# Kernel tuning notes

Hardware: AMD Instinct MI355X
Metric: run time of the kernel (lower is better)

The kernel has to match this reference:

```python
import jax, jax.numpy as jnp
import numpy as np

H, C = 3, 64          # heads, out_channels
NEG_SLOPE = 0.2       # PyG GATConv leaky_relu default
LN_EPS = 1e-5


def setup_inputs() -> dict:
    key = jax.random.key(0)
    ks = jax.random.split(key, 20)
    N, E, D_in, edge_dim = 50000, 800000, 64, 5
    g = lambda k, shape: (jax.random.normal(k, shape, dtype=jnp.float32) * 0.1)
    return {
        "x": jax.random.normal(ks[0], (N, D_in), dtype=jnp.float32),
        "edge_attr": jax.random.normal(ks[1], (E, edge_dim), dtype=jnp.float32),
        "lin_w": g(ks[2], (D_in, H * C)),          # GATConv.lin (bias=False)
        "att_src": g(ks[3], (H, C)),
        "att_dst": g(ks[4], (H, C)),
        "lin_edge_w": g(ks[5], (edge_dim, H * C)),  # GATConv.lin_edge (bias=False)
        "att_edge": g(ks[6], (H, C)),
        "gat_bias": jnp.zeros((H * C,), jnp.float32),
        "w1": g(ks[7], (H * C, C)),
        "b1": jnp.zeros((C,), jnp.float32),
        "ln1_g": jnp.ones((C,), jnp.float32),
        "ln1_b": jnp.zeros((C,), jnp.float32),
        "w2": g(ks[8], (C, C)),
        "b2": jnp.zeros((C,), jnp.float32),
        "ln2_g": jnp.ones((C,), jnp.float32),
        "ln2_b": jnp.zeros((C,), jnp.float32),
        "edge_index": jax.random.randint(ks[9], (2, E), 0, N),
    }


def layer_norm(x, g, b):
    m = jnp.mean(x, axis=-1, keepdims=True)
    v = jnp.mean((x - m) ** 2, axis=-1, keepdims=True)
    return (x - m) * jax.lax.rsqrt(v + LN_EPS) * g + b


def gat_conv(x, edge_index, edge_attr, lin_w, att_src, att_dst,
             lin_edge_w, att_edge, gat_bias):
    N = x.shape[0]
    src, dst = edge_index[0], edge_index[1]

    # add_self_loops=True with fill_value='mean': self-loop edge_attr is the
    # per-node mean of incoming edge attributes (0 if node has no in-edges).
    attr_sum = jax.ops.segment_sum(edge_attr, dst, num_segments=N)       # [N, edge_dim]
    cnt = jax.ops.segment_sum(jnp.ones((dst.shape[0],), edge_attr.dtype), dst, num_segments=N)
    loop_attr = attr_sum / jnp.maximum(cnt, 1.0)[:, None]
    loop = jnp.arange(N, dtype=src.dtype)
    src = jnp.concatenate([src, loop])
    dst = jnp.concatenate([dst, loop])
    ea = jnp.concatenate([edge_attr, loop_attr], axis=0)                  # [E2, edge_dim]

    xs = (x @ lin_w).reshape(N, H, C)                                     # [N, H, C]
    a_src = jnp.einsum('nhc,hc->nh', xs, att_src)                         # [N, H]
    a_dst = jnp.einsum('nhc,hc->nh', xs, att_dst)                         # [N, H]
    e = (ea @ lin_edge_w).reshape(-1, H, C)                               # [E2, H, C]
    a_edge = jnp.einsum('ehc,hc->eh', e, att_edge)                        # [E2, H]

    logits = a_src[src] + a_dst[dst] + a_edge                             # [E2, H]
    logits = jnp.where(logits >= 0, logits, NEG_SLOPE * logits)           # leaky_relu

    # segment softmax over incoming edges of each dst node (self loops ensure non-empty)
    lmax = jax.ops.segment_max(logits, dst, num_segments=N)               # [N, H]
    ex = jnp.exp(logits - lmax[dst])
    denom = jax.ops.segment_sum(ex, dst, num_segments=N)                  # [N, H]
    alpha = ex / denom[dst]                                               # [E2, H]

    msgs = alpha[:, :, None] * xs[src]                                    # [E2, H, C]
    out = jax.ops.segment_sum(msgs, dst, num_segments=N)                  # [N, H, C]
    return out.reshape(N, H * C) + gat_bias


def reference(x, edge_attr, lin_w, att_src, att_dst, lin_edge_w, att_edge,
              gat_bias, w1, b1, ln1_g, ln1_b, w2, b2, ln2_g, ln2_b, edge_index):
    x_gat = gat_conv(x, edge_index, edge_attr, lin_w, att_src, att_dst,
                     lin_edge_w, att_edge, gat_bias)
    x_gat = x_gat @ w1 + b1                         # linear1: [N, C]
    x_gat = layer_norm(x + x_gat, ln1_g, ln1_b)     # layerNorm1(x + x_gat)
    lin = x_gat @ w2 + b2                           # linear2
    out = layer_norm(lin + x_gat, ln2_g, ln2_b)     # layerNorm2(lin + x_gat)
    return out                                      # dropout p=0 -> identity
```

## Files before the change

### kernel.cpp

```cpp
#include <hip/hip_runtime.h>


#define HH 3
#define CC 64
#define DIN 64
#define ED 5
#define HC 192
#define NEG_SLOPE 0.2f
#define LN_EPS 1e-5f
#define LOG2E 1.44269504f

typedef __attribute__((ext_vector_type(8))) short bf16x8;
typedef __attribute__((ext_vector_type(4))) float f32x4;

__device__ __forceinline__ float leaky(float l) { return fmaxf(l, NEG_SLOPE * l); }

__device__ __forceinline__ unsigned short f2bf(float f) {
    unsigned u = __float_as_uint(f);
    unsigned r = (u + 0x7FFFu + ((u >> 16) & 1u)) >> 16;
    return (unsigned short)r;
}
__device__ __forceinline__ float bf2f(unsigned short u) {
    return __uint_as_float((unsigned)u << 16);
}
__device__ __forceinline__ float bf_lo(unsigned v) { return __uint_as_float(v << 16); }
__device__ __forceinline__ float bf_hi(unsigned v) { return __uint_as_float(v & 0xFFFF0000u); }

__device__ __forceinline__ bf16x8 pack8(float4 a, float4 b) {
    bf16x8 r;
    r[0] = (short)f2bf(a.x); r[1] = (short)f2bf(a.y);
    r[2] = (short)f2bf(a.z); r[3] = (short)f2bf(a.w);
    r[4] = (short)f2bf(b.x); r[5] = (short)f2bf(b.y);
    r[6] = (short)f2bf(b.z); r[7] = (short)f2bf(b.w);
    return r;
}

#define PREP_TOT (HC*DIN + DIN*HC + CC*CC + CC + ED*HH)
#define PREP_BLOCKS 30
__global__ __launch_bounds__(256) void k_prep_cnt(const float* __restrict__ lin_w,
                                                  const float* __restrict__ w1,
                                                  const float* __restrict__ w2,
                                                  const float* __restrict__ b1,
                                                  const float* __restrict__ gat_bias,
                                                  const float* __restrict__ lin_edge_w,
                                                  const float* __restrict__ att_edge,
                                                  unsigned short* __restrict__ linwt,
                                                  unsigned short* __restrict__ w1t,
                                                  unsigned short* __restrict__ w2t,
                                                  float* __restrict__ b1p,
                                                  float* __restrict__ we,
                                                  const int* __restrict__ ei,
                                                  int* __restrict__ icnt, int E) {
    if (blockIdx.x < PREP_BLOCKS) {
        for (int i = blockIdx.x * 256 + threadIdx.x; i < PREP_TOT; i += PREP_BLOCKS * 256) {
            if (i < HC * DIN) {
                int c = i >> 6, k = i & 63;
                linwt[i] = f2bf(lin_w[k * HC + c]);
            } else if (i < 2 * HC * DIN) {
                int j = i - HC * DIN;
                int c = j / HC, k = j - c * HC;
                w1t[j] = f2bf(w1[k * CC + c]);
            } else if (i < 2 * HC * DIN + CC * CC) {
                int j = i - 2 * HC * DIN;
                int c = j >> 6, k = j & 63;
                w2t[j] = f2bf(w2[k * CC + c]);
            } else if (i < 2 * HC * DIN + CC * CC + CC) {
                int c = i - (2 * HC * DIN + CC * CC);
                float s = b1[c];
                for (int k = 0; k < HC; ++k) s += gat_bias[k] * w1[k * CC + c];
                b1p[c] = s;
            } else {
                int q = i - (2 * HC * DIN + CC * CC + CC);
                int d = q / HH, h = q - d * HH;
                float s = 0.f;
                for (int c = 0; c < CC; ++c)
                    s += lin_edge_w[d * HC + h * CC + c] * att_edge[h * CC + c];
                we[q] = s * LOG2E;
            }
        }
    } else {
        int nb = gridDim.x - PREP_BLOCKS;
        for (int e = (blockIdx.x - PREP_BLOCKS) * 256 + threadIdx.x; e < E; e += nb * 256)
            atomicAdd(&icnt[ei[E + e]], 1);
    }
}

__global__ __launch_bounds__(256) void k_xs(const float* __restrict__ x,
                                            const unsigned short* __restrict__ linwt,
                                            const float* __restrict__ att_src,
                                            const float* __restrict__ att_dst,
                                            unsigned short* __restrict__ xsb,
                                            float* __restrict__ a_src,
                                            float* __restrict__ a_dst,
                                            const int* __restrict__ icnt,
                                            int* __restrict__ gtot,
                                            int* __restrict__ off,
                                            int* __restrict__ cursor,
                                            int N, int nbx) {
    __shared__ int wt[4];
    __shared__ int base_sh;
    if ((int)blockIdx.x >= nbx) {
        int bid = blockIdx.x - nbx;
        int i = bid * 256 + threadIdx.x;
        int lane = threadIdx.x & 63, wid = threadIdx.x >> 6;
        int v = (i < N) ? icnt[i] : 0;
        int incl = v;
        #pragma unroll
        for (int o = 1; o < 64; o <<= 1) {
            int u = __shfl_up(incl, o, 64);
            if (lane >= o) incl += u;
        }
        if (lane == 63) wt[wid] = incl;
        __syncthreads();
        if (threadIdx.x == 0)
            base_sh = atomicAdd(gtot, wt[0] + wt[1] + wt[2] + wt[3]);
        __syncthreads();
        int wpre = 0;
        for (int w2 = 0; w2 < wid; ++w2) wpre += wt[w2];
        int excl = base_sh + wpre + incl - v;
        if (i < N) { off[i] = excl; cursor[i] = excl; }
        return;
    }

    int lane = threadIdx.x & 63, w = threadIdx.x >> 6;
    int l15 = lane & 15, kg = (lane >> 4) * 8;
    int nb = blockIdx.x * 64;
    int arow = nb + w * 16 + l15;
    int arow_c = min(arow, N - 1);

    f32x4 acc[12];
    #pragma unroll
    for (int ct = 0; ct < 12; ++ct) acc[ct] = (f32x4){0.f, 0.f, 0.f, 0.f};

    #pragma unroll
    for (int k0 = 0; k0 < DIN; k0 += 32) {
        const float* ap = x + (size_t)arow_c * DIN + k0 + kg;
        float4 a0 = *(const float4*)ap;
        float4 a1 = *(const float4*)(ap + 4);
        bf16x8 af = pack8(a0, a1);
        #pragma unroll
        for (int ct = 0; ct < 12; ++ct) {
            bf16x8 bf = *(const bf16x8*)(linwt + (size_t)(ct * 16 + l15) * DIN + k0 + kg);
            acc[ct] = __builtin_amdgcn_mfma_f32_16x16x32_bf16(af, bf, acc[ct], 0, 0, 0);
        }
    }

    float asv[12], adv[12];
    #pragma unroll
    for (int ct = 0; ct < 12; ++ct) {
        int c = ct * 16 + l15;
        asv[ct] = att_src[c]; adv[ct] = att_dst[c];
    }

    int rbase = nb + w * 16 + (lane >> 4) * 4;
    #pragma unroll
    for (int j = 0; j < 4; ++j) {
        int r = rbase + j;
        bool ok = r < N;
        float ps0 = 0.f, ps1 = 0.f, ps2 = 0.f, pd0 = 0.f, pd1 = 0.f, pd2 = 0.f;
        #pragma unroll
        for (int ct = 0; ct < 12; ++ct) {
            float v = acc[ct][j];
            float s = v * asv[ct], d = v * adv[ct];
            if (ct < 4)      { ps0 += s; pd0 += d; }
            else if (ct < 8) { ps1 += s; pd1 += d; }
            else             { ps2 += s; pd2 += d; }
        }
        if (ok) {
            unsigned* row32 = (unsigned*)(xsb + (size_t)r * HC);
            #pragma unroll
            for (int ct = 0; ct < 4; ++ct) {
                int c = ct * 16 + l15;
                row32[c] = (unsigned)f2bf(acc[ct][j]) | ((unsigned)f2bf(acc[ct + 4][j]) << 16);
                xsb[(size_t)r * HC + 128 + c] = f2bf(acc[ct + 8][j]);
            }
        }
        #pragma unroll
        for (int o = 1; o < 16; o <<= 1) {
            ps0 += __shfl_xor(ps0, o, 64); pd0 += __shfl_xor(pd0, o, 64);
            ps1 += __shfl_xor(ps1, o, 64); pd1 += __shfl_xor(pd1, o, 64);
            ps2 += __shfl_xor(ps2, o, 64); pd2 += __shfl_xor(pd2, o, 64);
        }
        if (ok && l15 == 0) {
            a_src[r * HH + 0] = ps0 * LOG2E; a_src[r * HH + 1] = ps1 * LOG2E;
            a_src[r * HH + 2] = ps2 * LOG2E;
            a_dst[r * HH + 0] = pd0 * LOG2E; a_dst[r * HH + 1] = pd1 * LOG2E;
            a_dst[r * HH + 2] = pd2 * LOG2E;
        }
    }
}

__global__ __launch_bounds__(256) void k_fill(const float* __restrict__ ea,
                                              const int* __restrict__ ei,
                                              const float* __restrict__ a_src,
                                              const float* __restrict__ a_dst,
                                              const float* __restrict__ we,
                                              int* __restrict__ cursor,
                                              uint4* __restrict__ payload, int E) {
    int e = blockIdx.x * blockDim.x + threadIdx.x;
    if (e >= E) return;
    int s = ei[e], d = ei[E + e];
    int pos = atomicAdd(&cursor[d], 1);
    float attr[ED];
    #pragma unroll
    for (int j = 0; j < ED; ++j) attr[j] = ea[(size_t)e * ED + j];
    float aeh[HH], lp[HH];
    #pragma unroll
    for (int h = 0; h < HH; ++h) {
        float a = 0.f;
        #pragma unroll
        for (int j = 0; j < ED; ++j) a += attr[j] * we[j * HH + h];
        aeh[h] = a;
        lp[h] = a_src[s * HH + h] + a_dst[d * HH + h] + a;
    }
    uint4 pk;
    pk.x = (unsigned)f2bf(lp[0])  | ((unsigned)f2bf(lp[1])  << 16);
    pk.y = (unsigned)f2bf(lp[2])  | ((unsigned)f2bf(aeh[0]) << 16);
    pk.z = (unsigned)f2bf(aeh[1]) | ((unsigned)f2bf(aeh[2]) << 16);
    pk.w = (unsigned)s;
    payload[pos] = pk;
}

__global__ __launch_bounds__(256) void k_gat(const unsigned short* __restrict__ xsb,
                                             const float* __restrict__ a_src,
                                             const float* __restrict__ a_dst,
                                             const int* __restrict__ off,
                                             const int* __restrict__ icnt,
                                             const uint4* __restrict__ payload,
                                             unsigned short* __restrict__ oaccb, int N) {
    __shared__ float4 wbuf[4][64];
    int lane = threadIdx.x & 63;
    int wid  = threadIdx.x >> 6;
    const unsigned* xs32 = (const unsigned*)xsb;
    unsigned c128ml = 128u - (unsigned)lane;
    for (int n = blockIdx.x * 4 + wid; n < N; n += gridDim.x * 4) {
        int beg = off[n];
        int deg = icnt[n];

        float pden0 = 0.f, pden1 = 0.f, pden2 = 0.f;
        float pae0 = 0.f, pae1 = 0.f, pae2 = 0.f;
        float a0A = 0.f, a1A = 0.f, a2A = 0.f;
        float a0B = 0.f, a1B = 0.f, a2B = 0.f;

        for (int c0 = 0; c0 < deg; c0 += 64) {
            int cn = min(deg - c0, 64);
            float w0 = 0.f, w1 = 0.f, w2 = 0.f;
            int src = 0;
            if (lane < cn) {
                uint4 p = payload[beg + c0 + lane];
                w0 = exp2f(leaky(bf_lo(p.x)));
                w1 = exp2f(leaky(bf_hi(p.x)));
                w2 = exp2f(leaky(bf_lo(p.y)));
                pae0 += bf_hi(p.y);
                pae1 += bf_lo(p.z);
                pae2 += bf_hi(p.z);
                pden0 += w0; pden1 += w1; pden2 += w2;
                src = (int)p.w;
            }
            wbuf[wid][lane] = make_float4(w0, w1, w2, __int_as_float(src));
            int i = 0;
            for (; i + 2 <= cn; i += 2) {
                float4 ta = wbuf[wid][i];
                float4 tb = wbuf[wid][i + 1];
                unsigned ia = __umul24((unsigned)__float_as_int(ta.w), 96u) + lane;
                unsigned ib = __umul24((unsigned)__float_as_int(tb.w), 96u) + lane;
                unsigned va = xs32[ia];
                unsigned vb = xs32[ib];
                float xa2 = bf2f(xsb[(ia << 1) + c128ml]);
                float xb2 = bf2f(xsb[(ib << 1) + c128ml]);
                a0A += ta.x * bf_lo(va); a1A += ta.y * bf_hi(va); a2A += ta.z * xa2;
                a0B += tb.x * bf_lo(vb); a1B += tb.y * bf_hi(vb); a2B += tb.z * xb2;
            }
            if (i < cn) {
                float4 ta = wbuf[wid][i];
                unsigned ia = __umul24((unsigned)__float_as_int(ta.w), 96u) + lane;
                unsigned va = xs32[ia];
                a0A += ta.x * bf_lo(va);
                a1A += ta.y * bf_hi(va);
                a2A += ta.z * bf2f(xsb[(ia << 1) + c128ml]);
            }
        }

        #pragma unroll
        for (int o = 32; o; o >>= 1) {
            pden0 += __shfl_xor(pden0, o, 64);
            pden1 += __shfl_xor(pden1, o, 64);
            pden2 += __shfl_xor(pden2, o, 64);
            pae0  += __shfl_xor(pae0, o, 64);
            pae1  += __shfl_xor(pae1, o, 64);
            pae2  += __shfl_xor(pae2, o, 64);
        }

        float dc = fmaxf((float)deg, 1.0f);
        float inv_dc = __builtin_amdgcn_rcpf(dc);
        float sl0 = leaky(a_src[n * HH + 0] + a_dst[n * HH + 0] + pae0 * inv_dc);
        float sl1 = leaky(a_src[n * HH + 1] + a_dst[n * HH + 1] + pae1 * inv_dc);
        float sl2 = leaky(a_src[n * HH + 2] + a_dst[n * HH + 2] + pae2 * inv_dc);
        float e0 = exp2f(sl0), e1 = exp2f(sl1), e2 = exp2f(sl2);
        unsigned ian = __umul24((unsigned)n, 96u) + lane;
        unsigned van = xs32[ian];
        float xn2 = bf2f(xsb[(ian << 1) + c128ml]);
        float r0 = __builtin_amdgcn_rcpf(pden0 + e0);
        float r1 = __builtin_amdgcn_rcpf(pden1 + e1);
        float r2 = __builtin_amdgcn_rcpf(pden2 + e2);
        float acc0 = (a0A + a0B + e0 * bf_lo(van)) * r0;
        float acc1 = (a1A + a1B + e1 * bf_hi(van)) * r1;
        float acc2 = (a2A + a2B + e2 * xn2) * r2;
        size_t nbse = (size_t)n * HC;
        oaccb[nbse + 0 * CC + lane] = f2bf(acc0);
        oaccb[nbse + 1 * CC + lane] = f2bf(acc1);
        oaccb[nbse + 2 * CC + lane] = f2bf(acc2);
    }
}

__global__ __launch_bounds__(256) void k_mlp(const unsigned short* __restrict__ oaccb,
                                             const unsigned short* __restrict__ w1t,
                                             const unsigned short* __restrict__ w2t,
                                             const float* __restrict__ b1p,
                                             const float* __restrict__ x,
                                             const float* __restrict__ g1,
                                             const float* __restrict__ be1,
                                             const float* __restrict__ b2,
                                             const float* __restrict__ g2,
                                             const float* __restrict__ be2,
                                             float* __restrict__ out, int N) {
    __shared__ unsigned short H1[64 * 72];
    int lane = threadIdx.x & 63, w = threadIdx.x >> 6;
    int l15 = lane & 15, kg = (lane >> 4) * 8;
    int nb = blockIdx.x * 64;
    int arow = nb + w * 16 + l15;
    int arow_c = min(arow, N - 1);

    float c_b1[4], c_g1[4], c_be1[4], c_b2[4], c_g2[4], c_be2[4];
    #pragma unroll
    for (int ct = 0; ct < 4; ++ct) {
        int c = ct * 16 + l15;
        c_b1[ct] = b1p[c]; c_g1[ct] = g1[c]; c_be1[ct] = be1[c];
        c_b2[ct] = b2[c];  c_g2[ct] = g2[c]; c_be2[ct] = be2[c];
    }

    f32x4 acc[4];
    #pragma unroll
    for (int ct = 0; ct < 4; ++ct) acc[ct] = (f32x4){0.f, 0.f, 0.f, 0.f};
    #pragma unroll
    for (int k0 = 0; k0 < HC; k0 += 32) {
        bf16x8 af = *(const bf16x8*)(oaccb + (size_t)arow_c * HC + k0 + kg);
        #pragma unroll
        for (int ct = 0; ct < 4; ++ct) {
            bf16x8 bf = *(const bf16x8*)(w1t + (size_t)(ct * 16 + l15) * HC + k0 + kg);
            acc[ct] = __builtin_amdgcn_mfma_f32_16x16x32_bf16(af, bf, acc[ct], 0, 0, 0);
        }
    }

    int rbase = nb + w * 16 + (lane >> 4) * 4;
    int rloc0 = w * 16 + (lane >> 4) * 4;
    float h1v[4][4];
    float y[4][4];
    #pragma unroll
    for (int j = 0; j < 4; ++j) {
        int r = min(rbase + j, N - 1);
        #pragma unroll
        for (int ct = 0; ct < 4; ++ct)
            y[ct][j] = acc[ct][j] + c_b1[ct] + x[(size_t)r * DIN + ct * 16 + l15];
    }
    #pragma unroll
    for (int j = 0; j < 4; ++j) {
        float s = y[0][j] + y[1][j] + y[2][j] + y[3][j];
        #pragma unroll
        for (int o = 1; o < 16; o <<= 1) s += __shfl_xor(s, o, 64);
        float m = s * (1.0f / CC);
        float vs = 0.f;
        #pragma unroll
        for (int ct = 0; ct < 4; ++ct) { float d = y[ct][j] - m; vs += d * d; }
        #pragma unroll
        for (int o = 1; o < 16; o <<= 1) vs += __shfl_xor(vs, o, 64);
        float inv = rsqrtf(vs * (1.0f / CC) + LN_EPS);
        #pragma unroll
        for (int ct = 0; ct < 4; ++ct) {
            float h = (y[ct][j] - m) * inv * c_g1[ct] + c_be1[ct];
            h1v[ct][j] = h;
            H1[(rloc0 + j) * 72 + ct * 16 + l15] = f2bf(h);
        }
    }
    __syncthreads();

    f32x4 acc2[4];
    #pragma unroll
    for (int ct = 0; ct < 4; ++ct) acc2[ct] = (f32x4){0.f, 0.f, 0.f, 0.f};
    #pragma unroll
    for (int k0 = 0; k0 < CC; k0 += 32) {
        bf16x8 af = *(const bf16x8*)&H1[(w * 16 + l15) * 72 + k0 + kg];
        #pragma unroll
        for (int ct = 0; ct < 4; ++ct) {
            bf16x8 bf = *(const bf16x8*)(w2t + (size_t)(ct * 16 + l15) * CC + k0 + kg);
            acc2[ct] = __builtin_amdgcn_mfma_f32_16x16x32_bf16(af, bf, acc2[ct], 0, 0, 0);
        }
    }

    #pragma unroll
    for (int j = 0; j < 4; ++j) {
        float z0 = acc2[0][j] + c_b2[0] + h1v[0][j];
        float z1 = acc2[1][j] + c_b2[1] + h1v[1][j];
        float z2 = acc2[2][j] + c_b2[2] + h1v[2][j];
        float z3 = acc2[3][j] + c_b2[3] + h1v[3][j];
        float s = z0 + z1 + z2 + z3;
        #pragma unroll
        for (int o = 1; o < 16; o <<= 1) s += __shfl_xor(s, o, 64);
        float m = s * (1.0f / CC);
        float d0 = z0 - m, d1 = z1 - m, d2 = z2 - m, d3 = z3 - m;
        float vs = d0 * d0 + d1 * d1 + d2 * d2 + d3 * d3;
        #pragma unroll
        for (int o = 1; o < 16; o <<= 1) vs += __shfl_xor(vs, o, 64);
        float inv = rsqrtf(vs * (1.0f / CC) + LN_EPS);
        int r = rbase + j;
        if (r < N) {
            out[(size_t)r * CC + 0 * 16 + l15] = d0 * inv * c_g2[0] + c_be2[0];
            out[(size_t)r * CC + 1 * 16 + l15] = d1 * inv * c_g2[1] + c_be2[1];
            out[(size_t)r * CC + 2 * 16 + l15] = d2 * inv * c_g2[2] + c_be2[2];
            out[(size_t)r * CC + 3 * 16 + l15] = d3 * inv * c_g2[3] + c_be2[3];
        }
    }
}

extern "C" void kernel_launch(void* const* d_in, const int* in_sizes, int n_in,
                              void* d_out, int out_size, void* d_ws, size_t ws_size,
                              hipStream_t stream) {
    const float* x          = (const float*)d_in[0];
    const float* edge_attr  = (const float*)d_in[1];
    const float* lin_w      = (const float*)d_in[2];
    const float* att_src    = (const float*)d_in[3];
    const float* att_dst    = (const float*)d_in[4];
    const float* lin_edge_w = (const float*)d_in[5];
    const float* att_edge   = (const float*)d_in[6];
    const float* gat_bias   = (const float*)d_in[7];
    const float* w1         = (const float*)d_in[8];
    const float* b1         = (const float*)d_in[9];
    const float* ln1_g      = (const float*)d_in[10];
    const float* ln1_b      = (const float*)d_in[11];
    const float* w2         = (const float*)d_in[12];
    const float* b2         = (const float*)d_in[13];
    const float* ln2_g      = (const float*)d_in[14];
    const float* ln2_b      = (const float*)d_in[15];
    const int*   ei         = (const int*)d_in[16];
    float* out = (float*)d_out;

    const int N = in_sizes[0] / DIN;
    const int E = in_sizes[1] / ED;
    const int nb_scan = (N + 255) / 256;
    const int nbx = (N + 63) / 64;

    char* ws = (char*)d_ws;
    size_t off_b = 0;
    auto alloc = [&](size_t bytes) {
        size_t o = off_b;
        off_b = (off_b + bytes + 255) & ~(size_t)255;
        return o;
    };
    int* icnt = (int*)(ws + alloc((size_t)N * 4));
    int* gtot = (int*)(ws + alloc(4));
    size_t zero_bytes = off_b;
    unsigned short* xsb   = (unsigned short*)(ws + alloc((size_t)N * HC * 2));
    unsigned short* oaccb = (unsigned short*)(ws + alloc((size_t)N * HC * 2));
    float*  a_srcb  = (float*)(ws + alloc((size_t)N * HH * 4));
    float*  a_dstb  = (float*)(ws + alloc((size_t)N * HH * 4));
    int*    offb    = (int*)(ws + alloc((size_t)N * 4));
    int*    cursor  = (int*)(ws + alloc((size_t)N * 4));
    uint4*  payload = (uint4*)(ws + alloc((size_t)E * 16));
    unsigned short* linwt = (unsigned short*)(ws + alloc((size_t)HC * DIN * 2));
    unsigned short* w1t   = (unsigned short*)(ws + alloc((size_t)DIN * HC * 2));
    unsigned short* w2t   = (unsigned short*)(ws + alloc((size_t)CC * CC * 2));
    float* b1p = (float*)(ws + alloc((size_t)CC * 4));
    float* we  = (float*)(ws + alloc((size_t)ED * HH * 4));
    (void)ws_size; (void)n_in; (void)out_size;

    hipMemsetAsync(d_ws, 0, zero_bytes, stream);

    k_prep_cnt<<<PREP_BLOCKS + (E + 255) / 256, 256, 0, stream>>>(
        lin_w, w1, w2, b1, gat_bias, lin_edge_w, att_edge,
        linwt, w1t, w2t, b1p, we, ei, icnt, E);
    k_xs<<<nbx + nb_scan, 256, 0, stream>>>(x, linwt, att_src, att_dst, xsb,
                                            a_srcb, a_dstb, icnt, gtot, offb, cursor,
                                            N, nbx);
    k_fill<<<(E + 255) / 256, 256, 0, stream>>>(edge_attr, ei, a_srcb, a_dstb, we, cursor,
                                                payload, E);
    k_gat<<<(N + 3) / 4, 256, 0, stream>>>(xsb, a_srcb, a_dstb, offb, icnt, payload, oaccb, N);
    k_mlp<<<(N + 63) / 64, 256, 0, stream>>>(oaccb, w1t, w2t, b1p, x,
                                             ln1_g, ln1_b, b2, ln2_g, ln2_b, out, N);
}
```

Baseline: 184.9 us.

## Fuse GAT aggregation with MLP and layer norms in one kernel

```diff
diff --git a/kernel.cpp b/kernel.cpp
--- a/kernel.cpp
+++ b/kernel.cpp
@@ -221,204 +221,190 @@
     payload[pos] = pk;
 }
 
-__global__ __launch_bounds__(256) void k_gat(const unsigned short* __restrict__ xsb,
-                                             const float* __restrict__ a_src,
-                                             const float* __restrict__ a_dst,
-                                             const int* __restrict__ off,
-                                             const int* __restrict__ icnt,
-                                             const uint4* __restrict__ payload,
-                                             unsigned short* __restrict__ oaccb, int N) {
+__global__ __launch_bounds__(256) void k_gatmlp(const unsigned short* __restrict__ xsb,
+                                                const float* __restrict__ a_src,
+                                                const float* __restrict__ a_dst,
+                                                const int* __restrict__ off,
+                                                const int* __restrict__ icnt,
+                                                const uint4* __restrict__ payload,
+                                                const float* __restrict__ x,
+                                                const unsigned short* __restrict__ w1t,
+                                                const unsigned short* __restrict__ w2t,
+                                                const float* __restrict__ b1p,
+                                                const float* __restrict__ g1,
+                                                const float* __restrict__ be1,
+                                                const float* __restrict__ b2,
+                                                const float* __restrict__ g2,
+                                                const float* __restrict__ be2,
+                                                float* __restrict__ out, int N) {
     __shared__ float4 wbuf[4][64];
+    __shared__ unsigned short OA[16 * HC];
+    __shared__ unsigned short H1s[16 * 72];
+    __shared__ float red[2][4][16];
     int lane = threadIdx.x & 63;
     int wid  = threadIdx.x >> 6;
     const unsigned* xs32 = (const unsigned*)xsb;
     unsigned c128ml = 128u - (unsigned)lane;
-    for (int n = blockIdx.x * 4 + wid; n < N; n += gridDim.x * 4) {
-        int beg = off[n];
-        int deg = icnt[n];
-
-        float pden0 = 0.f, pden1 = 0.f, pden2 = 0.f;
-        float pae0 = 0.f, pae1 = 0.f, pae2 = 0.f;
-        float a0A = 0.f, a1A = 0.f, a2A = 0.f;
-        float a0B = 0.f, a1B = 0.f, a2B = 0.f;
-
-        for (int c0 = 0; c0 < deg; c0 += 64) {
-            int cn = min(deg - c0, 64);
-            float w0 = 0.f, w1 = 0.f, w2 = 0.f;
-            int src = 0;
-            if (lane < cn) {
-                uint4 p = payload[beg + c0 + lane];
-                w0 = exp2f(leaky(bf_lo(p.x)));
-                w1 = exp2f(leaky(bf_hi(p.x)));
-                w2 = exp2f(leaky(bf_lo(p.y)));
-                pae0 += bf_hi(p.y);
-                pae1 += bf_lo(p.z);
-                pae2 += bf_hi(p.z);
-                pden0 += w0; pden1 += w1; pden2 += w2;
-                src = (int)p.w;
+    int nb16 = blockIdx.x * 16;
+
+    #pragma unroll 1
+    for (int t = 0; t < 4; ++t) {
+        int row = wid * 4 + t;
+        int n = nb16 + row;
+        if (n < N) {
+            int beg = off[n];
+            int deg = icnt[n];
+            float pden0 = 0.f, pden1 = 0.f, pden2 = 0.f;
+            float pae0 = 0.f, pae1 = 0.f, pae2 = 0.f;
+            float a0A = 0.f, a1A = 0.f, a2A = 0.f;
+            float a0B = 0.f, a1B = 0.f, a2B = 0.f;
+
+            for (int c0 = 0; c0 < deg; c0 += 64) {
+                int cn = min(deg - c0, 64);
+                float w0 = 0.f, w1 = 0.f, w2 = 0.f;
+                int src = 0;
+                if (lane < cn) {
+                    uint4 p = payload[beg + c0 + lane];
+                    w0 = exp2f(leaky(bf_lo(p.x)));
+                    w1 = exp2f(leaky(bf_hi(p.x)));
+                    w2 = exp2f(leaky(bf_lo(p.y)));
+                    pae0 += bf_hi(p.y);
+                    pae1 += bf_lo(p.z);
+                    pae2 += bf_hi(p.z);
+                    pden0 += w0; pden1 += w1; pden2 += w2;
+                    src = (int)p.w;
+                }
+                wbuf[wid][lane] = make_float4(w0, w1, w2, __int_as_float(src));
+                int i = 0;
+                for (; i + 2 <= cn; i += 2) {
+                    float4 ta = wbuf[wid][i];
+                    float4 tb = wbuf[wid][i + 1];
+                    unsigned ia = __umul24((unsigned)__float_as_int(ta.w), 96u) + lane;
+                    unsigned ib = __umul24((unsigned)__float_as_int(tb.w), 96u) + lane;
+                    unsigned va = xs32[ia];
+                    unsigned vb = xs32[ib];
+                    float xa2 = bf2f(xsb[(ia << 1) + c128ml]);
+                    float xb2 = bf2f(xsb[(ib << 1) + c128ml]);
+                    a0A += ta.x * bf_lo(va); a1A += ta.y * bf_hi(va); a2A += ta.z * xa2;
+                    a0B += tb.x * bf_lo(vb); a1B += tb.y * bf_hi(vb); a2B += tb.z * xb2;
+                }
+                if (i < cn) {
+                    float4 ta = wbuf[wid][i];
+                    unsigned ia = __umul24((unsigned)__float_as_int(ta.w), 96u) + lane;
+                    unsigned va = xs32[ia];
+                    a0A += ta.x * bf_lo(va);
+                    a1A += ta.y * bf_hi(va);
+                    a2A += ta.z * bf2f(xsb[(ia << 1) + c128ml]);
+                }
             }
-            wbuf[wid][lane] = make_float4(w0, w1, w2, __int_as_float(src));
-            int i = 0;
-            for (; i + 2 <= cn; i += 2) {
-                float4 ta = wbuf[wid][i];
-                float4 tb = wbuf[wid][i + 1];
-                unsigned ia = __umul24((unsigned)__float_as_int(ta.w), 96u) + lane;
-                unsigned ib = __umul24((unsigned)__float_as_int(tb.w), 96u) + lane;
-                unsigned va = xs32[ia];
-                unsigned vb = xs32[ib];
-                float xa2 = bf2f(xsb[(ia << 1) + c128ml]);
-                float xb2 = bf2f(xsb[(ib << 1) + c128ml]);
-                a0A += ta.x * bf_lo(va); a1A += ta.y * bf_hi(va); a2A += ta.z * xa2;
-                a0B += tb.x * bf_lo(vb); a1B += tb.y * bf_hi(vb); a2B += tb.z * xb2;
+
+            #pragma unroll
+            for (int o = 32; o; o >>= 1) {
+                pden0 += __shfl_xor(pden0, o, 64);
+                pden1 += __shfl_xor(pden1, o, 64);
+                pden2 += __shfl_xor(pden2, o, 64);
+                pae0  += __shfl_xor(pae0, o, 64);
+                pae1  += __shfl_xor(pae1, o, 64);
+                pae2  += __shfl_xor(pae2, o, 64);
             }
-            if (i < cn) {
-                float4 ta = wbuf[wid][i];
-                unsigned ia = __umul24((unsigned)__float_as_int(ta.w), 96u) + lane;
-                unsigned va = xs32[ia];
-                a0A += ta.x * bf_lo(va);
-                a1A += ta.y * bf_hi(va);
-                a2A += ta.z * bf2f(xsb[(ia << 1) + c128ml]);
-            }
-        }
-
-        #pragma unroll
-        for (int o = 32; o; o >>= 1) {
-            pden0 += __shfl_xor(pden0, o, 64);
-            pden1 += __shfl_xor(pden1, o, 64);
-            pden2 += __shfl_xor(pden2, o, 64);
-            pae0  += __shfl_xor(pae0, o, 64);
-            pae1  += __shfl_xor(pae1, o, 64);
-            pae2  += __shfl_xor(pae2, o, 64);
-        }
-
-        float dc = fmaxf((float)deg, 1.0f);
-        float inv_dc = __builtin_amdgcn_rcpf(dc);
-        float sl0 = leaky(a_src[n * HH + 0] + a_dst[n * HH + 0] + pae0 * inv_dc);
-        float sl1 = leaky(a_src[n * HH + 1] + a_dst[n * HH + 1] + pae1 * inv_dc);
-        float sl2 = leaky(a_src[n * HH + 2] + a_dst[n * HH + 2] + pae2 * inv_dc);
-        float e0 = exp2f(sl0), e1 = exp2f(sl1), e2 = exp2f(sl2);
-        unsigned ian = __umul24((unsigned)n, 96u) + lane;
-        unsigned van = xs32[ian];
-        float xn2 = bf2f(xsb[(ian << 1) + c128ml]);
-        float r0 = __builtin_amdgcn_rcpf(pden0 + e0);
-        float r1 = __builtin_amdgcn_rcpf(pden1 + e1);
-        float r2 = __builtin_amdgcn_rcpf(pden2 + e2);
-        float acc0 = (a0A + a0B + e0 * bf_lo(van)) * r0;
-        float acc1 = (a1A + a1B + e1 * bf_hi(van)) * r1;
-        float acc2 = (a2A + a2B + e2 * xn2) * r2;
-        size_t nbse = (size_t)n * HC;
-        oaccb[nbse + 0 * CC + lane] = f2bf(acc0);
-        oaccb[nbse + 1 * CC + lane] = f2bf(acc1);
-        oaccb[nbse + 2 * CC + lane] = f2bf(acc2);
-    }
-}
-
-__global__ __launch_bounds__(256) void k_mlp(const unsigned short* __restrict__ oaccb,
-                                             const unsigned short* __restrict__ w1t,
-                                             const unsigned short* __restrict__ w2t,
-                                             const float* __restrict__ b1p,
-                                             const float* __restrict__ x,
-                                             const float* __restrict__ g1,
-                                             const float* __restrict__ be1,
-                                             const float* __restrict__ b2,
-                                             const float* __restrict__ g2,
-                                             const float* __restrict__ be2,
-                                             float* __restrict__ out, int N) {
-    __shared__ unsigned short H1[64 * 72];
-    int lane = threadIdx.x & 63, w = threadIdx.x >> 6;
+
+            float dc = fmaxf((float)deg, 1.0f);
+            float inv_dc = __builtin_amdgcn_rcpf(dc);
+            float sl0 = leaky(a_src[n * HH + 0] + a_dst[n * HH + 0] + pae0 * inv_dc);
+            float sl1 = leaky(a_src[n * HH + 1] + a_dst[n * HH + 1] + pae1 * inv_dc);
+            float sl2 = leaky(a_src[n * HH + 2] + a_dst[n * HH + 2] + pae2 * inv_dc);
+            float e0 = exp2f(sl0), e1 = exp2f(sl1), e2 = exp2f(sl2);
+            unsigned ian = __umul24((unsigned)n, 96u) + lane;
+            unsigned van = xs32[ian];
+            float xn2 = bf2f(xsb[(ian << 1) + c128ml]);
+            float r0 = __builtin_amdgcn_rcpf(pden0 + e0);
+            float r1 = __builtin_amdgcn_rcpf(pden1 + e1);
+            float r2 = __builtin_amdgcn_rcpf(pden2 + e2);
+            OA[row * HC +       lane] = f2bf((a0A + a0B + e0 * bf_lo(van)) * r0);
+            OA[row * HC +  64 + lane] = f2bf((a1A + a1B + e1 * bf_hi(van)) * r1);
+            OA[row * HC + 128 + lane] = f2bf((a2A + a2B + e2 * xn2) * r2);
+        } else {
+            OA[row * HC +       lane] = 0;
+            OA[row * HC +  64 + lane] = 0;
+            OA[row * HC + 128 + lane] = 0;
+        }
+    }
+    __syncthreads();
+
     int l15 = lane & 15, kg = (lane >> 4) * 8;
-    int nb = blockIdx.x * 64;
-    int arow = nb + w * 16 + l15;
-    int arow_c = min(arow, N - 1);
-
-    float c_b1[4], c_g1[4], c_be1[4], c_b2[4], c_g2[4], c_be2[4];
-    #pragma unroll
-    for (int ct = 0; ct < 4; ++ct) {
-        int c = ct * 16 + l15;
-        c_b1[ct] = b1p[c]; c_g1[ct] = g1[c]; c_be1[ct] = be1[c];
-        c_b2[ct] = b2[c];  c_g2[ct] = g2[c]; c_be2[ct] = be2[c];
-    }
-
-    f32x4 acc[4];
-    #pragma unroll
-    for (int ct = 0; ct < 4; ++ct) acc[ct] = (f32x4){0.f, 0.f, 0.f, 0.f};
+    int col = wid * 16 + l15;
+    float cb1 = b1p[col], cg1 = g1[col], cbe1 = be1[col];
+    float cb2 = b2[col],  cg2 = g2[col], cbe2 = be2[col];
+
+    f32x4 acc = (f32x4){0.f, 0.f, 0.f, 0.f};
     #pragma unroll
     for (int k0 = 0; k0 < HC; k0 += 32) {
-        bf16x8 af = *(const bf16x8*)(oaccb + (size_t)arow_c * HC + k0 + kg);
-        #pragma unroll
-        for (int ct = 0; ct < 4; ++ct) {
-            bf16x8 bf = *(const bf16x8*)(w1t + (size_t)(ct * 16 + l15) * HC + k0 + kg);
-            acc[ct] = __builtin_amdgcn_mfma_f32_16x16x32_bf16(af, bf, acc[ct], 0, 0, 0);
-        }
-    }
-
-    int rbase = nb + w * 16 + (lane >> 4) * 4;
-    int rloc0 = w * 16 + (lane >> 4) * 4;
-    float h1v[4][4];
-    float y[4][4];
+        bf16x8 af = *(const bf16x8*)&OA[l15 * HC + k0 + kg];
+        bf16x8 bf = *(const bf16x8*)(w1t + (size_t)col * HC + k0 + kg);
+        acc = __builtin_amdgcn_mfma_f32_16x16x32_bf16(af, bf, acc, 0, 0, 0);
+    }
+
+    int rj0 = (lane >> 4) * 4;
+    float y[4], h1v[4];
     #pragma unroll
     for (int j = 0; j < 4; ++j) {
-        int r = min(rbase + j, N - 1);
-        #pragma unroll
-        for (int ct = 0; ct < 4; ++ct)
-            y[ct][j] = acc[ct][j] + c_b1[ct] + x[(size_t)r * DIN + ct * 16 + l15];
-    }
+        int r = min(nb16 + rj0 + j, N - 1);
+        y[j] = acc[j] + cb1 + x[(size_t)r * DIN + col];
+        float s = y[j], q = y[j] * y[j];
+        #pragma unroll
+        for (int o = 1; o < 16; o <<= 1) {
+            s += __shfl_xor(s, o, 64);
+            q += __shfl_xor(q, o, 64);
+        }
+        if (l15 == 0) { red[0][wid][rj0 + j] = s; red[1][wid][rj0 + j] = q; }
+    }
+    __syncthreads();
     #pragma unroll
     for (int j = 0; j < 4; ++j) {
-        float s = y[0][j] + y[1][j] + y[2][j] + y[3][j];
-        #pragma unroll
-        for (int o = 1; o < 16; o <<= 1) s += __shfl_xor(s, o, 64);
+        int rj = rj0 + j;
+        float s = red[0][0][rj] + red[0][1][rj] + red[0][2][rj] + red[0][3][rj];
+        float q = red[1][0][rj] + red[1][1][rj] + red[1][2][rj] + red[1][3][rj];
         float m = s * (1.0f / CC);
-        float vs = 0.f;
-        #pragma unroll
-        for (int ct = 0; ct < 4; ++ct) { float d = y[ct][j] - m; vs += d * d; }
-        #pragma unroll
-        for (int o = 1; o < 16; o <<= 1) vs += __shfl_xor(vs, o, 64);
-        float inv = rsqrtf(vs * (1.0f / CC) + LN_EPS);
-        #pragma unroll
-        for (int ct = 0; ct < 4; ++ct) {
-            float h = (y[ct][j] - m) * inv * c_g1[ct] + c_be1[ct];
-            h1v[ct][j] = h;
-            H1[(rloc0 + j) * 72 + ct * 16 + l15] = f2bf(h);
-        }
+        float var = q * (1.0f / CC) - m * m;
+        float inv = rsqrtf(var + LN_EPS);
+        float h = (y[j] - m) * inv * cg1 + cbe1;
+        h1v[j] = h;
+        H1s[rj * 72 + col] = f2bf(h);
     }
     __syncthreads();
 
-    f32x4 acc2[4];
-    #pragma unroll
-    for (int ct = 0; ct < 4; ++ct) acc2[ct] = (f32x4){0.f, 0.f, 0.f, 0.f};
+    f32x4 acc2 = (f32x4){0.f, 0.f, 0.f, 0.f};
     #pragma unroll
     for (int k0 = 0; k0 < CC; k0 += 32) {
-        bf16x8 af = *(const bf16x8*)&H1[(w * 16 + l15) * 72 + k0 + kg];
-        #pragma unroll
-        for (int ct = 0; ct < 4; ++ct) {
-            bf16x8 bf = *(const bf16x8*)(w2t + (size_t)(ct * 16 + l15) * CC + k0 + kg);
-            acc2[ct] = __builtin_amdgcn_mfma_f32_16x16x32_bf16(af, bf, acc2[ct], 0, 0, 0);
-        }
-    }
-
+        bf16x8 af = *(const bf16x8*)&H1s[l15 * 72 + k0 + kg];
+        bf16x8 bf = *(const bf16x8*)(w2t + (size_t)col * CC + k0 + kg);
+        acc2 = __builtin_amdgcn_mfma_f32_16x16x32_bf16(af, bf, acc2, 0, 0, 0);
+    }
+
+    float z[4];
     #pragma unroll
     for (int j = 0; j < 4; ++j) {
-        float z0 = acc2[0][j] + c_b2[0] + h1v[0][j];
-        float z1 = acc2[1][j] + c_b2[1] + h1v[1][j];
-        float z2 = acc2[2][j] + c_b2[2] + h1v[2][j];
-        float z3 = acc2[3][j] + c_b2[3] + h1v[3][j];
-        float s = z0 + z1 + z2 + z3;
-        #pragma unroll
-        for (int o = 1; o < 16; o <<= 1) s += __shfl_xor(s, o, 64);
+        z[j] = acc2[j] + cb2 + h1v[j];
+        float s = z[j], q = z[j] * z[j];
+        #pragma unroll
+        for (int o = 1; o < 16; o <<= 1) {
+            s += __shfl_xor(s, o, 64);
+            q += __shfl_xor(q, o, 64);
+        }
+        if (l15 == 0) { red[0][wid][rj0 + j] = s; red[1][wid][rj0 + j] = q; }
+    }
+    __syncthreads();
+    #pragma unroll
+    for (int j = 0; j < 4; ++j) {
+        int rj = rj0 + j;
+        float s = red[0][0][rj] + red[0][1][rj] + red[0][2][rj] + red[0][3][rj];
+        float q = red[1][0][rj] + red[1][1][rj] + red[1][2][rj] + red[1][3][rj];
         float m = s * (1.0f / CC);
-        float d0 = z0 - m, d1 = z1 - m, d2 = z2 - m, d3 = z3 - m;
-        float vs = d0 * d0 + d1 * d1 + d2 * d2 + d3 * d3;
-        #pragma unroll
-        for (int o = 1; o < 16; o <<= 1) vs += __shfl_xor(vs, o, 64);
-        float inv = rsqrtf(vs * (1.0f / CC) + LN_EPS);
-        int r = rbase + j;
-        if (r < N) {
-            out[(size_t)r * CC + 0 * 16 + l15] = d0 * inv * c_g2[0] + c_be2[0];
-            out[(size_t)r * CC + 1 * 16 + l15] = d1 * inv * c_g2[1] + c_be2[1];
-            out[(size_t)r * CC + 2 * 16 + l15] = d2 * inv * c_g2[2] + c_be2[2];
-            out[(size_t)r * CC + 3 * 16 + l15] = d3 * inv * c_g2[3] + c_be2[3];
-        }
+        float var = q * (1.0f / CC) - m * m;
+        float inv = rsqrtf(var + LN_EPS);
+        int r = nb16 + rj;
+        if (r < N)
+            out[(size_t)r * CC + col] = (z[j] - m) * inv * cg2 + cbe2;
     }
 }
 
@@ -459,8 +445,7 @@
     int* icnt = (int*)(ws + alloc((size_t)N * 4));
     int* gtot = (int*)(ws + alloc(4));
     size_t zero_bytes = off_b;
-    unsigned short* xsb   = (unsigned short*)(ws + alloc((size_t)N * HC * 2));
-    unsigned short* oaccb = (unsigned short*)(ws + alloc((size_t)N * HC * 2));
+    unsigned short* xsb = (unsigned short*)(ws + alloc((size_t)N * HC * 2));
     float*  a_srcb  = (float*)(ws + alloc((size_t)N * HH * 4));
     float*  a_dstb  = (float*)(ws + alloc((size_t)N * HH * 4));
     int*    offb    = (int*)(ws + alloc((size_t)N * 4));
@@ -483,7 +468,7 @@
                                             N, nbx);
     k_fill<<<(E + 255) / 256, 256, 0, stream>>>(edge_attr, ei, a_srcb, a_dstb, we, cursor,
                                                 payload, E);
-    k_gat<<<(N + 3) / 4, 256, 0, stream>>>(xsb, a_srcb, a_dstb, offb, icnt, payload, oaccb, N);
-    k_mlp<<<(N + 63) / 64, 256, 0, stream>>>(oaccb, w1t, w2t, b1p, x,
-                                             ln1_g, ln1_b, b2, ln2_g, ln2_b, out, N);
-}
+    k_gatmlp<<<(N + 15) / 16, 256, 0, stream>>>(xsb, a_srcb, a_dstb, offb, icnt, payload,
+                                                x, w1t, w2t, b1p, ln1_g, ln1_b,
+                                                b2, ln2_g, ln2_b, out, N);
+}
```

Measured after the change: 184.1 us. About the same (-0.4%).
